# Performance work log

Measured on AMD Instinct MI355X. Metric: run time of the kernel, lower is better.

## Reference

```python
import jax, jax.numpy as jnp
import numpy as np

EMBED = 1024
HEADS = 16
HEAD_DIM = EMBED // HEADS


def setup_inputs() -> dict:
    key = jax.random.key(0)
    k1, k2, k3, k4, k5 = jax.random.split(key, 5)
    N, S = 2, 2048
    values = jax.random.normal(k1, (N, S, EMBED), dtype=jnp.float32)
    keys = jax.random.normal(k2, (N, S, EMBED), dtype=jnp.float32)
    query = jax.random.normal(k3, (N, S, EMBED), dtype=jnp.float32)
    mask = jnp.ones((N, 1, S, S), dtype=jnp.int32)
    # fc_out: Linear(heads*head_dim, embed_size) with bias; torch stores W as [out, in]
    W_out = jax.random.normal(k4, (EMBED, EMBED), dtype=jnp.float32) / np.sqrt(EMBED)
    b_out = jax.random.normal(k5, (EMBED,), dtype=jnp.float32) * 0.01
    return {"values": values, "keys": keys, "query": query, "mask": mask,
            "W_out": W_out, "b_out": b_out}


def reference(values, keys, query, mask, W_out, b_out):
    N, S, E = query.shape
    H, D = HEADS, HEAD_DIM
    # NOTE: source module never applies its q/k/v Linear layers (bug preserved).
    v = values.reshape(N, S, H, D)
    k = keys.reshape(N, S, H, D)
    q = query.reshape(N, S, H, D)
    energy = jnp.einsum('nqhd,nkhd->nhqk', q, k)  # [N,H,S,S]
    energy = jnp.where(mask == 0, jnp.float32(-1e20), energy)
    # non-standard scale: sqrt(embed_size), faithful to source
    attn = jax.nn.softmax(energy / jnp.sqrt(jnp.float32(E)), axis=3)
    out = jnp.einsum('nhql,nlhd->nqhd', attn, v).reshape(N, S, H * D)
    return out @ W_out.T + b_out
```

## Files before the change

### kernel.cpp

```cpp
#include <hip/hip_runtime.h>
#include <stdint.h>

#define S_LEN 2048
#define EMB 1024
#define NHEADS 16
#define HD 64
#define LOG2E 1.4426950408889634f

typedef __bf16 bf16x8 __attribute__((ext_vector_type(8)));
typedef float f32x4 __attribute__((ext_vector_type(4)));
typedef unsigned short u16;

#define MFMA16(a, b, c) __builtin_amdgcn_mfma_f32_16x16x32_bf16(a, b, c, 0, 0, 0)
#define GLOAD_LDS16(gp, lp)                                        \
  __builtin_amdgcn_global_load_lds(                                \
      (const __attribute__((address_space(1))) unsigned int*)(gp), \
      (__attribute__((address_space(3))) unsigned int*)(lp), 16, 0, 0)

__device__ __forceinline__ u16 bf16r(float x) {
  union { float f; unsigned int u; } c; c.f = x;
  unsigned int u = c.u + 0x7fffu + ((c.u >> 16) & 1u);
  return (u16)(u >> 16);
}

__device__ __forceinline__ unsigned int cvt_pk_bf16(float lo, float hi) {
  unsigned int r;
  asm("v_cvt_pk_bf16_f32 %0, %1, %2" : "=v"(r) : "v"(lo), "v"(hi));
  return r;
}

__device__ __forceinline__ float fexp2(float x) {
  float r;
  asm("v_exp_f32 %0, %1" : "=v"(r) : "v"(x));
  return r;
}

__device__ __forceinline__ int kperm(int k) {
  int kb = (k >> 4) & 3, g = (k >> 2) & 3, r = k & 3;
  return (kb >> 1) * 32 + g * 8 + (kb & 1) * 4 + r;
}

__global__ __launch_bounds__(256) void prep_kernel(
    const float* __restrict__ values, const float* __restrict__ keys,
    const float* __restrict__ W, const int* __restrict__ mask,
    u16* __restrict__ vt, u16* __restrict__ kb, u16* __restrict__ wb,
    unsigned char* __restrict__ fl2) {
  __shared__ u16 tile[64][65];
  __shared__ int s_ok[4];
  int b = blockIdx.x;
  int t = threadIdx.x;
  if (b < 1024) {
    int st = b & 31, h = (b >> 5) & 15, n = b >> 9;
    int s0 = st * 64;
    int d = t & 63, r4 = t >> 6;
#pragma unroll
    for (int i = 0; i < 16; ++i) {
      int s = r4 + i * 4;
      float x = values[(size_t)(n * S_LEN + s0 + s) * EMB + h * HD + d];
      tile[s][d] = bf16r(x);
    }
    __syncthreads();
    int sp = s0 + kperm(d);
#pragma unroll
    for (int i = 0; i < 16; ++i) {
      int dd = r4 + i * 4;
      vt[(size_t)((n * NHEADS + h) * HD + dd) * S_LEN + sp] = tile[d][dd];
    }
  } else if (b < 2048) {
    int idx = (b - 1024) * 256 + t;
    const float4* in4 = (const float4*)keys;
    ushort4* out4 = (ushort4*)kb;
#pragma unroll
    for (int j = 0; j < 4; ++j) {
      float4 v = in4[idx + j * 262144];
      ushort4 o;
      o.x = bf16r(v.x); o.y = bf16r(v.y); o.z = bf16r(v.z); o.w = bf16r(v.w);
      out4[idx + j * 262144] = o;
    }
  } else if (b < 2304) {
    int idx = (b - 2048) * 256 + t;
    const float4* in4 = (const float4*)W;
    ushort4* out4 = (ushort4*)wb;
#pragma unroll
    for (int j = 0; j < 4; ++j) {
      float4 v = in4[idx + j * 65536];
      ushort4 o;
      o.x = bf16r(v.x); o.y = bf16r(v.y); o.z = bf16r(v.z); o.w = bf16r(v.w);
      out4[idx + j * 65536] = o;
    }
  } else {
    int idx = b - 2304;
    int kt = idx & 31, qt = (idx >> 5) & 15, n = idx >> 9;
    int qr = t >> 1, c8 = t & 1;
    const int4* mp = (const int4*)(mask + (size_t)n * S_LEN * S_LEN +
                                   (size_t)(qt * 128 + qr) * S_LEN + kt * 64) + c8 * 8;
    int ok = 1;
#pragma unroll
    for (int i = 0; i < 8; ++i) {
      int4 m = mp[i];
      ok &= (m.x != 0) & (m.y != 0) & (m.z != 0) & (m.w != 0);
    }
    ok = __all(ok);
    if ((t & 63) == 0) s_ok[t >> 6] = ok;
    __syncthreads();
    if (t == 0) fl2[idx] = (unsigned char)(s_ok[0] & s_ok[1] & s_ok[2] & s_ok[3]);
  }
}

__global__ __launch_bounds__(256, 2) void attn_kernel(
    const float* __restrict__ query, const u16* __restrict__ kbuf,
    const u16* __restrict__ vt, const int* __restrict__ mask,
    const unsigned char* __restrict__ fl2, u16* __restrict__ ob) {
  __shared__ __align__(16) unsigned char kl[2][8192];
  __shared__ __align__(16) unsigned char vl[2][8192];

  int b = blockIdx.x;
  b = (b & 7) * 64 + (b >> 3);
  int qt = b & 15, h = (b >> 4) & 15, n = b >> 8;
  int t = threadIdx.x, w = t >> 6, l = t & 63, l16 = l & 15, g = l >> 4;
  int q0 = qt * 128 + w * 32;

  const float QS = 0.03125f * LOG2E;
  bf16x8 aq[2][2];
#pragma unroll
  for (int u = 0; u < 2; ++u)
#pragma unroll
    for (int hh = 0; hh < 2; ++hh) {
      const float* qp = query + (size_t)(n * S_LEN + q0 + u * 16 + l16) * EMB +
                        h * HD + hh * 32 + g * 8;
      float4 f0 = *(const float4*)qp;
      float4 f1 = *(const float4*)(qp + 4);
      union { bf16x8 v; unsigned int u32[4]; } qq;
      qq.u32[0] = cvt_pk_bf16(f0.x * QS, f0.y * QS);
      qq.u32[1] = cvt_pk_bf16(f0.z * QS, f0.w * QS);
      qq.u32[2] = cvt_pk_bf16(f1.x * QS, f1.y * QS);
      qq.u32[3] = cvt_pk_bf16(f1.z * QS, f1.w * QS);
      aq[u][hh] = qq.v;
    }

  f32x4 zero4 = {0.f, 0.f, 0.f, 0.f};
  f32x4 acc[2][4];
  float lrun[2] = {0.f, 0.f}, mrun[2] = {0.f, 0.f};
#pragma unroll
  for (int u = 0; u < 2; ++u)
#pragma unroll
    for (int db = 0; db < 4; ++db) acc[u][db] = zero4;

  int row_s = t >> 3, cc = t & 7;
  int sc = cc ^ (row_s & 7);
  const u16* gk0 = kbuf + (size_t)(n * S_LEN + row_s) * EMB + h * HD + sc * 8;
  const u16* gv0 = vt + (size_t)((n * NHEADS + h) * HD + row_s) * S_LEN + sc * 8;

  auto stage = [&](int kt, int nb) {
    const u16* gk = gk0 + (size_t)kt * 64 * EMB;
    const u16* gv = gv0 + kt * 64;
    GLOAD_LDS16(gk, kl[nb] + (w * 64) * 16);
    GLOAD_LDS16(gk + 32 * EMB, kl[nb] + (256 + w * 64) * 16);
    GLOAD_LDS16(gv, vl[nb] + (w * 64) * 16);
    GLOAD_LDS16(gv + 32 * S_LEN, vl[nb] + (256 + w * 64) * 16);
  };

  stage(0, 0);
  __syncthreads();

  for (int kt = 0; kt < S_LEN / 64; ++kt) {
    int cur = kt & 1;
    if (kt + 1 < S_LEN / 64) stage(kt + 1, cur ^ 1);
    const unsigned char* kc = kl[cur];
    const unsigned char* vc = vl[cur];

    f32x4 sf[2][4];
    __builtin_amdgcn_s_setprio(1);
#pragma unroll
    for (int kb = 0; kb < 4; ++kb) {
      int row = kb * 16 + l16;
      const unsigned char* kr = kc + row * 128;
      int sw = (row & 7) << 4;
      bf16x8 bk0 = *(const bf16x8*)(kr + ((g * 16) ^ sw));
      bf16x8 bk1 = *(const bf16x8*)(kr + ((64 + g * 16) ^ sw));
#pragma unroll
      for (int u = 0; u < 2; ++u) {
        f32x4 z = zero4;
        z = MFMA16(bk0, aq[u][0], z);
        z = MFMA16(bk1, aq[u][1], z);
        sf[u][kb] = z;
      }
    }
    __builtin_amdgcn_s_setprio(0);

    unsigned char fflag = fl2[((n * 16 + qt) * 32) + kt];
    if (!fflag) {
#pragma unroll
      for (int u = 0; u < 2; ++u) {
        const int* mrow = mask + (size_t)n * S_LEN * S_LEN +
                          (size_t)(q0 + u * 16 + l16) * S_LEN + kt * 64 + g * 4;
#pragma unroll
        for (int kb = 0; kb < 4; ++kb) {
          int4 mm = *(const int4*)(mrow + kb * 16);
          if (mm.x == 0) sf[u][kb][0] = -100.f;
          if (mm.y == 0) sf[u][kb][1] = -100.f;
          if (mm.z == 0) sf[u][kb][2] = -100.f;
          if (mm.w == 0) sf[u][kb][3] = -100.f;
        }
      }
    }

    bf16x8 pa[2][2];
#pragma unroll
    for (int u = 0; u < 2; ++u) {
      float lmax = sf[u][0][0];
#pragma unroll
      for (int kb = 0; kb < 4; ++kb)
#pragma unroll
        for (int r = 0; r < 4; ++r) lmax = fmaxf(lmax, sf[u][kb][r]);
      if (!__all(lmax <= mrun[u] + 8.f)) {
        float rmax = fmaxf(lmax, __shfl_xor(lmax, 16));
        rmax = fmaxf(rmax, __shfl_xor(rmax, 32));
        float Mn = fmaxf(mrun[u], rmax);
        float corr = fexp2(mrun[u] - Mn);
        mrun[u] = Mn;
        lrun[u] *= corr;
#pragma unroll
        for (int r = 0; r < 4; ++r) {
          float ca = __shfl(corr, (l & 48) + (g << 2) + r);
#pragma unroll
          for (int db = 0; db < 4; ++db) acc[u][db][r] *= ca;
        }
      }
      float p[4][4];
#pragma unroll
      for (int kb = 0; kb < 4; ++kb)
#pragma unroll
        for (int r = 0; r < 4; ++r)
          p[kb][r] = fexp2(sf[u][kb][r] - mrun[u]);
      float s01 = (p[0][0] + p[0][1]) + (p[0][2] + p[0][3]);
      float s23 = (p[1][0] + p[1][1]) + (p[1][2] + p[1][3]);
      float s45 = (p[2][0] + p[2][1]) + (p[2][2] + p[2][3]);
      float s67 = (p[3][0] + p[3][1]) + (p[3][2] + p[3][3]);
      lrun[u] += (s01 + s23) + (s45 + s67);
#pragma unroll
      for (int hh = 0; hh < 2; ++hh) {
        union { bf16x8 v; unsigned int u32[4]; } pp;
        pp.u32[0] = cvt_pk_bf16(p[2 * hh][0], p[2 * hh][1]);
        pp.u32[1] = cvt_pk_bf16(p[2 * hh][2], p[2 * hh][3]);
        pp.u32[2] = cvt_pk_bf16(p[2 * hh + 1][0], p[2 * hh + 1][1]);
        pp.u32[3] = cvt_pk_bf16(p[2 * hh + 1][2], p[2 * hh + 1][3]);
        pa[u][hh] = pp.v;
      }
    }

    __builtin_amdgcn_s_setprio(1);
#pragma unroll
    for (int hh = 0; hh < 2; ++hh)
#pragma unroll
      for (int db = 0; db < 4; ++db) {
        int d = db * 16 + l16;
        bf16x8 bv = *(const bf16x8*)(vc + d * 128 + ((hh * 64 + g * 16) ^ ((d & 7) << 4)));
        acc[0][db] = MFMA16(pa[0][hh], bv, acc[0][db]);
        acc[1][db] = MFMA16(pa[1][hh], bv, acc[1][db]);
      }
    __builtin_amdgcn_s_setprio(0);

    __syncthreads();
  }

#pragma unroll
  for (int u = 0; u < 2; ++u) {
    float s = lrun[u];
    s += __shfl_xor(s, 16);
    s += __shfl_xor(s, 32);
    float rinv[4];
#pragma unroll
    for (int r = 0; r < 4; ++r) {
      float sr = __shfl(s, (l & 48) + (g << 2) + r);
      rinv[r] = 1.f / sr;
    }
#pragma unroll
    for (int db = 0; db < 4; ++db)
#pragma unroll
      for (int r = 0; r < 4; ++r) {
        int qg = q0 + u * 16 + (g << 2) + r;
        ob[(size_t)(n * S_LEN + qg) * EMB + h * HD + db * 16 + l16] =
            bf16r(acc[u][db][r] * rinv[r]);
      }
  }
}

__global__ __launch_bounds__(256) void proj_kernel(
    const u16* __restrict__ A, const u16* __restrict__ Bt,
    const float* __restrict__ bias, float* __restrict__ C) {
  __shared__ __align__(16) unsigned char al[2][16384];
  __shared__ __align__(16) unsigned char bl[2][8192];
  int bm = blockIdx.x, bn = blockIdx.y;
  int t = threadIdx.x, w = t >> 6, l = t & 63;
  int l16 = l & 15, g = l >> 4;
  f32x4 zero4 = {0.f, 0.f, 0.f, 0.f};
  f32x4 acc[2][4];
#pragma unroll
  for (int mi = 0; mi < 2; ++mi)
#pragma unroll
    for (int nj = 0; nj < 4; ++nj) acc[mi][nj] = zero4;
  int row_s = t >> 3, cc = t & 7;
  int sc = cc ^ (row_s & 7);
  const u16* ga0 = A + (size_t)(bm * 128 + row_s) * EMB + sc * 8;
  const u16* gb0 = Bt + (size_t)(bn * 64 + row_s) * EMB + sc * 8;

  auto stage = [&](int ks, int nb) {
#pragma unroll
    for (int i = 0; i < 4; ++i)
      GLOAD_LDS16(ga0 + (size_t)i * 32 * EMB + ks * 64, al[nb] + (i * 256 + w * 64) * 16);
#pragma unroll
    for (int i = 0; i < 2; ++i)
      GLOAD_LDS16(gb0 + (size_t)i * 32 * EMB + ks * 64, bl[nb] + (i * 256 + w * 64) * 16);
  };

  stage(0, 0);
  __syncthreads();

  for (int ks = 0; ks < 16; ++ks) {
    int cur = ks & 1;
    if (ks + 1 < 16) stage(ks + 1, cur ^ 1);
    __builtin_amdgcn_s_setprio(1);
#pragma unroll
    for (int hh = 0; hh < 2; ++hh) {
      bf16x8 af[2], bfr[4];
#pragma unroll
      for (int mi = 0; mi < 2; ++mi) {
        int row = w * 32 + mi * 16 + l16;
        af[mi] = *(const bf16x8*)(al[cur] + row * 128 + ((hh * 64 + g * 16) ^ ((row & 7) << 4)));
      }
#pragma unroll
      for (int nj = 0; nj < 4; ++nj) {
        int row = nj * 16 + l16;
        bfr[nj] = *(const bf16x8*)(bl[cur] + row * 128 + ((hh * 64 + g * 16) ^ ((row & 7) << 4)));
      }
#pragma unroll
      for (int mi = 0; mi < 2; ++mi)
#pragma unroll
        for (int nj = 0; nj < 4; ++nj) acc[mi][nj] = MFMA16(af[mi], bfr[nj], acc[mi][nj]);
    }
    __builtin_amdgcn_s_setprio(0);
    __syncthreads();
  }
#pragma unroll
  for (int nj = 0; nj < 4; ++nj) {
    int j = bn * 64 + nj * 16 + l16;
    float bj = bias[j];
#pragma unroll
    for (int mi = 0; mi < 2; ++mi) {
      int i0 = bm * 128 + w * 32 + mi * 16 + g * 4;
#pragma unroll
      for (int r = 0; r < 4; ++r) C[(size_t)(i0 + r) * EMB + j] = acc[mi][nj][r] + bj;
    }
  }
}

extern "C" void kernel_launch(void* const* d_in, const int* in_sizes, int n_in,
                              void* d_out, int out_size, void* d_ws, size_t ws_size,
                              hipStream_t stream) {
  const float* values = (const float*)d_in[0];
  const float* keys = (const float*)d_in[1];
  const float* query = (const float*)d_in[2];
  const int* mask = (const int*)d_in[3];
  const float* W = (const float*)d_in[4];
  const float* bias = (const float*)d_in[5];
  float* out = (float*)d_out;

  u16* kb = (u16*)d_ws;
  u16* vt = kb + 4194304;
  u16* ob = vt + 4194304;
  u16* wb = ob + 4194304;
  unsigned char* fl2 = (unsigned char*)(wb + 1048576);

  prep_kernel<<<3328, 256, 0, stream>>>(values, keys, W, mask, vt, kb, wb, fl2);
  attn_kernel<<<512, 256, 0, stream>>>(query, kb, vt, mask, fl2, ob);
  proj_kernel<<<dim3(32, 16), 256, 0, stream>>>(ob, wb, bias, out);
}
```

Before: 90.23 us.

## Split attention key range across two blocks and merge with a combine kernel

Splits the key dimension of attention into two halves handled by separate blocks (flash-decoding style split-K), doubling the grid from 512 to 1024 blocks and raising the launch-bounds occupancy hint. Each half writes unnormalized fp32 partial outputs plus running max and sum, and a new combine kernel rescales and merges them into the bf16 buffer consumed by the projection. The aim is better CU occupancy, since 512 blocks underfill the GPU. The cost is an extra kernel launch and a roundtrip of fp32 partials through global memory (about 32 MB written and read).

```diff
diff --git a/kernel.cpp b/kernel.cpp
--- a/kernel.cpp
+++ b/kernel.cpp
@@ -6,6 +6,7 @@
 #define NHEADS 16
 #define HD 64
 #define LOG2E 1.4426950408889634f
+#define NROWS 65536
 
 typedef __bf16 bf16x8 __attribute__((ext_vector_type(8)));
 typedef float f32x4 __attribute__((ext_vector_type(4)));
@@ -107,18 +108,20 @@
   }
 }
 
-__global__ __launch_bounds__(256, 2) void attn_kernel(
+__global__ __launch_bounds__(256, 4) void attn_kernel(
     const float* __restrict__ query, const u16* __restrict__ kbuf,
     const u16* __restrict__ vt, const int* __restrict__ mask,
-    const unsigned char* __restrict__ fl2, u16* __restrict__ ob) {
+    const unsigned char* __restrict__ fl2, float* __restrict__ po,
+    float2* __restrict__ ml) {
   __shared__ __align__(16) unsigned char kl[2][8192];
   __shared__ __align__(16) unsigned char vl[2][8192];
 
   int b = blockIdx.x;
-  b = (b & 7) * 64 + (b >> 3);
-  int qt = b & 15, h = (b >> 4) & 15, n = b >> 8;
+  b = (b & 7) * 128 + (b >> 3);
+  int qt = b & 15, half = (b >> 4) & 1, h = (b >> 5) & 15, n = b >> 9;
   int t = threadIdx.x, w = t >> 6, l = t & 63, l16 = l & 15, g = l >> 4;
   int q0 = qt * 128 + w * 32;
+  int kt0 = half * 16;
 
   const float QS = 0.03125f * LOG2E;
   bf16x8 aq[2][2];
@@ -160,12 +163,12 @@
     GLOAD_LDS16(gv + 32 * S_LEN, vl[nb] + (256 + w * 64) * 16);
   };
 
-  stage(0, 0);
+  stage(kt0, 0);
   __syncthreads();
 
-  for (int kt = 0; kt < S_LEN / 64; ++kt) {
+  for (int kt = kt0; kt < kt0 + 16; ++kt) {
     int cur = kt & 1;
-    if (kt + 1 < S_LEN / 64) stage(kt + 1, cur ^ 1);
+    if (kt + 1 < kt0 + 16) stage(kt + 1, cur ^ 1);
     const unsigned char* kc = kl[cur];
     const unsigned char* vc = vl[cur];
 
@@ -264,25 +267,47 @@
     __syncthreads();
   }
 
+  size_t rowbase = (size_t)(n * NHEADS + h) * S_LEN + q0;
 #pragma unroll
   for (int u = 0; u < 2; ++u) {
     float s = lrun[u];
     s += __shfl_xor(s, 16);
     s += __shfl_xor(s, 32);
-    float rinv[4];
-#pragma unroll
-    for (int r = 0; r < 4; ++r) {
-      float sr = __shfl(s, (l & 48) + (g << 2) + r);
-      rinv[r] = 1.f / sr;
+    if (g == 0) {
+      float2 v; v.x = mrun[u]; v.y = s;
+      ml[(size_t)half * NROWS + rowbase + u * 16 + l16] = v;
     }
 #pragma unroll
     for (int db = 0; db < 4; ++db)
 #pragma unroll
       for (int r = 0; r < 4; ++r) {
-        int qg = q0 + u * 16 + (g << 2) + r;
-        ob[(size_t)(n * S_LEN + qg) * EMB + h * HD + db * 16 + l16] =
-            bf16r(acc[u][db][r] * rinv[r]);
-      }
+        size_t rq = rowbase + u * 16 + (g << 2) + r;
+        po[((size_t)half * NROWS + rq) * HD + db * 16 + l16] = acc[u][db][r];
+      }
+  }
+}
+
+__global__ __launch_bounds__(256) void combine_kernel(
+    const float* __restrict__ po, const float2* __restrict__ ml,
+    u16* __restrict__ ob) {
+  int idx = blockIdx.x * 256 + threadIdx.x;
+  int stride = gridDim.x * 256;
+  for (; idx < NROWS * 16; idx += stride) {
+    int row = idx >> 4, d4 = idx & 15;
+    float2 a = ml[row], b = ml[NROWS + row];
+    float m = fmaxf(a.x, b.x);
+    float c0 = fexp2(a.x - m), c1 = fexp2(b.x - m);
+    float rinv = 1.f / (a.y * c0 + b.y * c1);
+    c0 *= rinv; c1 *= rinv;
+    float4 o0 = ((const float4*)po)[(size_t)row * 16 + d4];
+    float4 o1 = ((const float4*)po)[(size_t)NROWS * 16 + (size_t)row * 16 + d4];
+    ushort4 o;
+    o.x = bf16r(o0.x * c0 + o1.x * c1);
+    o.y = bf16r(o0.y * c0 + o1.y * c1);
+    o.z = bf16r(o0.z * c0 + o1.z * c1);
+    o.w = bf16r(o0.w * c0 + o1.w * c1);
+    int n = row >> 15, h = (row >> 11) & 15, q = row & 2047;
+    *(ushort4*)(ob + (size_t)(n * S_LEN + q) * EMB + h * HD + d4 * 4) = o;
   }
 }
 
@@ -371,8 +396,11 @@
   u16* ob = vt + 4194304;
   u16* wb = ob + 4194304;
   unsigned char* fl2 = (unsigned char*)(wb + 1048576);
+  float* po = (float*)(fl2 + 65536);
+  float2* ml = (float2*)(po + 2 * (size_t)NROWS * HD);
 
   prep_kernel<<<3328, 256, 0, stream>>>(values, keys, W, mask, vt, kb, wb, fl2);
-  attn_kernel<<<512, 256, 0, stream>>>(query, kb, vt, mask, fl2, ob);
+  attn_kernel<<<1024, 256, 0, stream>>>(query, kb, vt, mask, fl2, po, ml);
+  combine_kernel<<<2048, 256, 0, stream>>>(po, ml, ob);
   proj_kernel<<<dim3(32, 16), 256, 0, stream>>>(ob, wb, bias, out);
 }
```

Result: slower. 92.60 us (+2.6%).
